# Optimization experiments

Hardware: AMD Instinct MI355X
Metric: run time of the kernel (lower is better)

The kernel has to match this reference:

```python
import jax, jax.numpy as jnp
import numpy as np

L = 65536      # number of received symbols
MT = 64        # Mtestangles
NF = 64        # averaging half-window -> filter length 2*NF+1 = 129


def setup_inputs() -> dict:
    key = jax.random.key(0)
    k1, k2 = jax.random.split(key, 2)
    # 64-QAM constellation, unit average power
    pts = jnp.arange(-7, 8, 2, dtype=jnp.float32)  # 8 PAM levels
    re, im = jnp.meshgrid(pts, pts, indexing='ij')
    sym = (re + 1j * im).reshape(-1)
    sym = sym / jnp.sqrt(jnp.mean(jnp.abs(sym) ** 2))
    # received signal: random constellation symbols + slow phase drift + noise
    idx = jax.random.randint(k1, (L,), 0, sym.shape[0])
    drift = jnp.cumsum(0.002 * jax.random.normal(k2, (L,), jnp.float32))
    noise = 0.05 * (jax.random.normal(jax.random.fold_in(key, 7), (L,), jnp.float32)
                    + 1j * jax.random.normal(jax.random.fold_in(key, 8), (L,), jnp.float32))
    x = sym[idx] * jnp.exp(1j * drift) + noise
    # triangular averaging filter: [1..N+1, N..1]
    avg_filter = jnp.concatenate([
        jnp.arange(1, NF + 2, dtype=jnp.float32),
        jnp.arange(NF, 0, -1, dtype=jnp.float32)])
    return {
        'x_real': x.real.astype(jnp.float32),
        'x_imag': x.imag.astype(jnp.float32),
        'symbols_real': sym.real.astype(jnp.float32),
        'symbols_imag': sym.imag.astype(jnp.float32),
        'avg_filter': avg_filter,
        'temperature': jnp.array([0.05], dtype=jnp.float32),
    }


def reference(x_real, x_imag, symbols_real, symbols_imag, avg_filter, temperature):
    # angles for no_sectors==4: linspace(-pi/4, pi/4 - (pi/2)/M, M)
    angles = jnp.linspace(-np.pi / 4, np.pi / 4 - (np.pi / 2) / MT, MT).astype(jnp.float32)  # [M]
    x = jax.lax.complex(x_real, x_imag)                       # [L]
    EE = x[:, None] * jnp.exp(1j * angles)                    # [L, M] rotated copies
    # dist[l,m] = min_s |EE - s|^2 = |x|^2 + min_s(|s|^2 - 2 Re(EE conj(s)))
    sym_sq = symbols_real ** 2 + symbols_imag ** 2            # [S]
    cross = EE.real[:, :, None] * symbols_real + EE.imag[:, :, None] * symbols_imag  # [L, M, S]
    dist = (x_real ** 2 + x_imag ** 2)[:, None] + jnp.min(sym_sq - 2.0 * cross, axis=2)  # [L, M]
    # sliding-window average along time (torch conv1d padding='same', normalized taps)
    w = avg_filter / jnp.sum(avg_filter)                      # [2N+1]
    mvg = jax.lax.conv_general_dilated(
        dist.T[:, None, :],            # [M, 1, L]
        w[None, None, :],              # [1, 1, 2N+1]
        window_strides=(1,), padding=[(NF, NF)],
        dimension_numbers=('NCH', 'OIH', 'NCH'))[:, 0, :].T   # [L, M]
    mvg = mvg / jnp.sum(mvg, axis=1, keepdims=True)
    # softmin over test angles
    smvg = jax.nn.softmax(-mvg / temperature[0], axis=1)      # [L, M]
    sang = 4.0 * angles
    ang = jnp.arctan2(smvg @ jnp.sin(sang), smvg @ jnp.cos(sang))  # [L]
    ph = jnp.unwrap(ang, discont=np.pi, period=2 * np.pi) / 4.0
    out = x * jnp.exp(1j * ph)
    return out, ph
```

## Files before the change

### kernel.cpp

```cpp
#include <hip/hip_runtime.h>


#define LN   65536
#define PI_F 3.14159265358979323846f
#define TWO_PI_F 6.2831853071795864769f

#define CORR(dd) (((dd) < -PI_F) ? 1 : (((dd) > PI_F) ? -1 : 0))

__global__ __launch_bounds__(512) void v14_stage_ang(const float* __restrict__ xr,
                                                     const float* __restrict__ xi,
                                                     const float* __restrict__ temp,
                                                     float* __restrict__ ang_out) {
    __shared__ float P1[64 * 257];
    __shared__ float xsr[256], xsi[256];
    __shared__ float tot1[8][64];
    __shared__ float tot2[8][64];
    __shared__ float s4v[64], c4v[64];

    const int t   = threadIdx.x;
    const int l0  = blockIdx.x * 128;
    const int m   = t & 63;
    const int seg = t >> 6;

    if (t < 256) {
        int gl = l0 - 64 + t;
        bool ok = (unsigned)gl < (unsigned)LN;
        xsr[t] = ok ? xr[gl] : 0.0f;
        xsi[t] = ok ? xi[gl] : 0.0f;
    }
    if (t >= 448) {
        int mm = t - 448;
        float a4 = (float)mm * (PI_F / 32.0f) - PI_F;
        float s, c; sincosf(a4, &s, &c);
        s4v[mm] = s; c4v[mm] = c;
    }
    __syncthreads();

    {
        const float am = (float)m * (PI_F / 128.0f) - (PI_F * 0.25f);
        float sm, cm; sincosf(am, &sm, &cm);
        const float SQ = 6.4807406984078602f;
        const float cq = cm * SQ, sq = sm * SQ;
        float pr[32];
        float p = 0.0f;
        #pragma unroll
        for (int i = 0; i < 32; ++i) {
            int li = seg * 32 + i;
            float a = xsr[li], b = xsi[li];
            float tr = a * cq - b * sq;
            float ti = a * sq + b * cq;
            float rr = fminf(fmaxf(rintf(fmaf(tr, 0.5f, 3.5f)), 0.0f), 7.0f);
            float ri = fminf(fmaxf(rintf(fmaf(ti, 0.5f, 3.5f)), 0.0f), 7.0f);
            float dr = fmaf(-2.0f, rr, tr + 7.0f);
            float di = fmaf(-2.0f, ri, ti + 7.0f);
            float d = fmaf(dr, dr, di * di) * (1.0f / 42.0f);
            d = ((unsigned)(l0 - 64 + li) < (unsigned)LN) ? d : 0.0f;
            p += d;
            pr[i] = p;
        }
        tot1[seg][m] = p;
        __syncthreads();
        float off = 0.0f;
        #pragma unroll
        for (int s = 0; s < 7; ++s) if (s < seg) off += tot1[s][m];
        #pragma unroll
        for (int i = 0; i < 32; ++i) P1[m * 257 + seg * 32 + i] = pr[i] + off;
    }
    __syncthreads();

    const int j0 = seg * 25;
    const int jn = (seg < 7) ? 25 : 18;
    {
        float q[25];
        float p2 = 0.0f;
        #pragma unroll
        for (int i = 0; i < 25; ++i) {
            if (i < jn) {
                int j = j0 + i;
                float hi = P1[m * 257 + 63 + j];
                float lo = (j >= 2) ? P1[m * 257 + j - 2] : 0.0f;
                p2 += hi - lo;
                q[i] = p2;
            }
        }
        tot2[seg][m] = p2;
        __syncthreads();
        float off2 = 0.0f;
        #pragma unroll
        for (int s = 0; s < 7; ++s) if (s < seg) off2 += tot2[s][m];
        float* Q = P1;
        #pragma unroll
        for (int i = 0; i < 25; ++i) if (i < jn) Q[m * 195 + j0 + i] = q[i] + off2;
    }
    __syncthreads();

    {
        const float* Q = P1;
        const float T = temp[0];
        const int sub = t & 3;
        const int r   = t >> 2;
        const int mb  = sub * 16;

        float v[16];
        float rs = 0.0f, mn = 3.4e38f;
        #pragma unroll
        for (int i = 0; i < 16; ++i) {
            int mm = mb + i;
            float vv = Q[mm * 195 + r + 65] - Q[mm * 195 + r];
            v[i] = vv; rs += vv; mn = fminf(mn, vv);
        }
        rs += __shfl_xor(rs, 1, 64); rs += __shfl_xor(rs, 2, 64);
        mn = fminf(mn, __shfl_xor(mn, 1, 64)); mn = fminf(mn, __shfl_xor(mn, 2, 64));

        float inv = 1.0f / (rs * T);
        float ss = 0.0f, sc = 0.0f;
        #pragma unroll
        for (int i = 0; i < 16; ++i) {
            int mm = mb + i;
            float e = __expf((mn - v[i]) * inv);
            ss = fmaf(e, s4v[mm], ss);
            sc = fmaf(e, c4v[mm], sc);
        }
        ss += __shfl_xor(ss, 1, 64); ss += __shfl_xor(ss, 2, 64);
        sc += __shfl_xor(sc, 1, 64); sc += __shfl_xor(sc, 2, 64);
        if (sub == 0) ang_out[l0 + r] = atan2f(ss, sc);
    }
}

__global__ __launch_bounds__(256) void v14_scan_out(const float* __restrict__ xr,
                                                    const float* __restrict__ xi,
                                                    const float* __restrict__ ang,
                                                    int* __restrict__ partial,
                                                    int* __restrict__ flags,
                                                    float* __restrict__ out_base) {
    __shared__ int wtot[4];
    __shared__ int s_boff;
    const int t = threadIdx.x;
    const int b = blockIdx.x;
    const int e = b * 256 + t;
    const int i4 = e * 4;

    float4 a = *(const float4*)(ang + i4);
    float prev = (i4 == 0) ? 0.0f : ang[i4 - 1];

    int s0 = CORR(a.x - prev);
    int s1 = CORR(a.y - a.x);
    int s2 = CORR(a.z - a.y);
    int s3 = CORR(a.w - a.z);
    int k0 = s0, k1 = k0 + s1, k2 = k1 + s2, k3 = k2 + s3;

    const int lane = t & 63, wv = t >> 6;
    int scan = k3;
    #pragma unroll
    for (int off = 1; off < 64; off <<= 1) {
        int v = __shfl_up(scan, off, 64);
        if (lane >= off) scan += v;
    }
    if (lane == 63) wtot[wv] = scan;
    __syncthreads();
    int woff = 0;
    #pragma unroll
    for (int j = 0; j < 3; ++j) if (j < wv) woff += wtot[j];
    const int excl = woff + scan - k3;

    if (t == 0) {
        int btot = wtot[0] + wtot[1] + wtot[2] + wtot[3];
        __hip_atomic_store(&partial[b], btot, __ATOMIC_RELAXED, __HIP_MEMORY_SCOPE_AGENT);
        __hip_atomic_store(&flags[b], 1, __ATOMIC_RELEASE, __HIP_MEMORY_SCOPE_AGENT);
    }
    if (t < 64) {
        int v = 0;
        if (t < b) {
            while (__hip_atomic_load(&flags[t], __ATOMIC_ACQUIRE, __HIP_MEMORY_SCOPE_AGENT) != 1) {}
            v = __hip_atomic_load(&partial[t], __ATOMIC_RELAXED, __HIP_MEMORY_SCOPE_AGENT);
        }
        #pragma unroll
        for (int off = 1; off < 64; off <<= 1) v += __shfl_xor(v, off, 64);
        if (t == 0) s_boff = v;
    }
    __syncthreads();
    const int boff = s_boff;

    float4 xa = *(const float4*)(xr + i4);
    float4 xb = *(const float4*)(xi + i4);
    float ph0 = (a.x + TWO_PI_F * (float)(boff + excl + k0)) * 0.25f;
    float ph1 = (a.y + TWO_PI_F * (float)(boff + excl + k1)) * 0.25f;
    float ph2 = (a.z + TWO_PI_F * (float)(boff + excl + k2)) * 0.25f;
    float ph3 = (a.w + TWO_PI_F * (float)(boff + excl + k3)) * 0.25f;
    float s0f, c0f, s1f, c1f, s2f, c2f, s3f, c3f;
    sincosf(ph0, &s0f, &c0f); sincosf(ph1, &s1f, &c1f);
    sincosf(ph2, &s2f, &c2f); sincosf(ph3, &s3f, &c3f);
    float4 re = make_float4(xa.x * c0f - xb.x * s0f, xa.y * c1f - xb.y * s1f,
                            xa.z * c2f - xb.z * s2f, xa.w * c3f - xb.w * s3f);
    *(float4*)(out_base + i4)      = re;
    *(float4*)(out_base + LN + i4) = make_float4(ph0, ph1, ph2, ph3);
}

extern "C" void kernel_launch(void* const* d_in, const int* in_sizes, int n_in,
                              void* d_out, int out_size, void* d_ws, size_t ws_size,
                              hipStream_t stream) {
    (void)in_sizes; (void)n_in; (void)out_size; (void)ws_size;
    const float* xr   = (const float*)d_in[0];
    const float* xi   = (const float*)d_in[1];
    const float* temp = (const float*)d_in[5];

    float* ang     = (float*)d_ws;
    int*   partial = (int*)((char*)d_ws + LN * sizeof(float));
    int*   flags   = (int*)((char*)d_ws + LN * sizeof(float) + 256);

    v14_stage_ang<<<LN / 128, 512, 0, stream>>>(xr, xi, temp, ang);
    v14_scan_out <<<64, 256, 0, stream>>>(xr, xi, ang, partial, flags, (float*)d_out);
}
```

Measured before the change: 76.71 us.

## Fuse angle stage and unwrap scan into one kernel with per-block lookback

Merges the angle-estimation kernel and the unwrap/rotate kernel into a single launch. Each block computes one extra halo angle so the unwrap difference at the block boundary is computed locally. Cross-block offsets come from a decoupled lookback over 512 block partials. This removes the second launch and the intermediate angle buffer, at the risk of serialized spin-waiting across many blocks and reliance on forward-progress scheduling.

```diff
diff --git a/kernel.cpp b/kernel.cpp
--- a/kernel.cpp
+++ b/kernel.cpp
@@ -7,23 +7,29 @@
 
 #define CORR(dd) (((dd) < -PI_F) ? 1 : (((dd) > PI_F) ? -1 : 0))
 
-__global__ __launch_bounds__(512) void v14_stage_ang(const float* __restrict__ xr,
-                                                     const float* __restrict__ xi,
-                                                     const float* __restrict__ temp,
-                                                     float* __restrict__ ang_out) {
-    __shared__ float P1[64 * 257];
-    __shared__ float xsr[256], xsi[256];
+__global__ __launch_bounds__(512) void v15_fused(const float* __restrict__ xr,
+                                                 const float* __restrict__ xi,
+                                                 const float* __restrict__ temp,
+                                                 int* __restrict__ partial,
+                                                 int* __restrict__ flags,
+                                                 float* __restrict__ out_base) {
+    __shared__ float P1[64 * 258];
+    __shared__ float xsr[260], xsi[260];
     __shared__ float tot1[8][64];
     __shared__ float tot2[8][64];
     __shared__ float s4v[64], c4v[64];
+    __shared__ float ang_lds[129];
+    __shared__ int   wtot[2];
+    __shared__ int   s_boff;
 
     const int t   = threadIdx.x;
-    const int l0  = blockIdx.x * 128;
+    const int b   = blockIdx.x;
+    const int l0  = b * 128;
     const int m   = t & 63;
     const int seg = t >> 6;
 
-    if (t < 256) {
-        int gl = l0 - 64 + t;
+    if (t < 257) {
+        int gl = l0 - 65 + t;
         bool ok = (unsigned)gl < (unsigned)LN;
         xsr[t] = ok ? xr[gl] : 0.0f;
         xsi[t] = ok ? xi[gl] : 0.0f;
@@ -41,22 +47,26 @@
         float sm, cm; sincosf(am, &sm, &cm);
         const float SQ = 6.4807406984078602f;
         const float cq = cm * SQ, sq = sm * SQ;
-        float pr[32];
+        const int li0 = seg * 33;
+        const int rn  = (seg < 7) ? 33 : 26;
+        float pr[33];
         float p = 0.0f;
         #pragma unroll
-        for (int i = 0; i < 32; ++i) {
-            int li = seg * 32 + i;
-            float a = xsr[li], b = xsi[li];
-            float tr = a * cq - b * sq;
-            float ti = a * sq + b * cq;
-            float rr = fminf(fmaxf(rintf(fmaf(tr, 0.5f, 3.5f)), 0.0f), 7.0f);
-            float ri = fminf(fmaxf(rintf(fmaf(ti, 0.5f, 3.5f)), 0.0f), 7.0f);
-            float dr = fmaf(-2.0f, rr, tr + 7.0f);
-            float di = fmaf(-2.0f, ri, ti + 7.0f);
-            float d = fmaf(dr, dr, di * di) * (1.0f / 42.0f);
-            d = ((unsigned)(l0 - 64 + li) < (unsigned)LN) ? d : 0.0f;
-            p += d;
-            pr[i] = p;
+        for (int i = 0; i < 33; ++i) {
+            if (i < rn) {
+                int li = li0 + i;
+                float a = xsr[li], bb = xsi[li];
+                float tr = a * cq - bb * sq;
+                float ti = a * sq + bb * cq;
+                float rr = fminf(fmaxf(rintf(fmaf(tr, 0.5f, 3.5f)), 0.0f), 7.0f);
+                float ri = fminf(fmaxf(rintf(fmaf(ti, 0.5f, 3.5f)), 0.0f), 7.0f);
+                float dr = fmaf(-2.0f, rr, tr + 7.0f);
+                float di = fmaf(-2.0f, ri, ti + 7.0f);
+                float d = fmaf(dr, dr, di * di) * (1.0f / 42.0f);
+                d = ((unsigned)(l0 - 65 + li) < (unsigned)LN) ? d : 0.0f;
+                p += d;
+                pr[i] = p;
+            }
         }
         tot1[seg][m] = p;
         __syncthreads();
@@ -64,21 +74,21 @@
         #pragma unroll
         for (int s = 0; s < 7; ++s) if (s < seg) off += tot1[s][m];
         #pragma unroll
-        for (int i = 0; i < 32; ++i) P1[m * 257 + seg * 32 + i] = pr[i] + off;
-    }
-    __syncthreads();
-
-    const int j0 = seg * 25;
-    const int jn = (seg < 7) ? 25 : 18;
+        for (int i = 0; i < 33; ++i) if (i < rn) P1[m * 258 + li0 + i] = pr[i] + off;
+    }
+    __syncthreads();
+
     {
+        const int j0 = seg * 25;
+        const int jn = (j0 < 193) ? ((193 - j0 < 25) ? (193 - j0) : 25) : 0;
         float q[25];
         float p2 = 0.0f;
         #pragma unroll
         for (int i = 0; i < 25; ++i) {
             if (i < jn) {
                 int j = j0 + i;
-                float hi = P1[m * 257 + 63 + j];
-                float lo = (j >= 2) ? P1[m * 257 + j - 2] : 0.0f;
+                float hi = P1[m * 258 + j + 64];
+                float lo = (j >= 1) ? P1[m * 258 + j - 1] : 0.0f;
                 p2 += hi - lo;
                 q[i] = p2;
             }
@@ -97,103 +107,89 @@
     {
         const float* Q = P1;
         const float T = temp[0];
-        const int sub = t & 3;
-        const int r   = t >> 2;
-        const int mb  = sub * 16;
-
-        float v[16];
-        float rs = 0.0f, mn = 3.4e38f;
-        #pragma unroll
-        for (int i = 0; i < 16; ++i) {
-            int mm = mb + i;
-            float vv = Q[mm * 195 + r + 65] - Q[mm * 195 + r];
-            v[i] = vv; rs += vv; mn = fminf(mn, vv);
-        }
-        rs += __shfl_xor(rs, 1, 64); rs += __shfl_xor(rs, 2, 64);
-        mn = fminf(mn, __shfl_xor(mn, 1, 64)); mn = fminf(mn, __shfl_xor(mn, 2, 64));
-
-        float inv = 1.0f / (rs * T);
-        float ss = 0.0f, sc = 0.0f;
-        #pragma unroll
-        for (int i = 0; i < 16; ++i) {
-            int mm = mb + i;
-            float e = __expf((mn - v[i]) * inv);
-            ss = fmaf(e, s4v[mm], ss);
-            sc = fmaf(e, c4v[mm], sc);
-        }
-        ss += __shfl_xor(ss, 1, 64); ss += __shfl_xor(ss, 2, 64);
-        sc += __shfl_xor(sc, 1, 64); sc += __shfl_xor(sc, 2, 64);
-        if (sub == 0) ang_out[l0 + r] = atan2f(ss, sc);
-    }
-}
-
-__global__ __launch_bounds__(256) void v14_scan_out(const float* __restrict__ xr,
-                                                    const float* __restrict__ xi,
-                                                    const float* __restrict__ ang,
-                                                    int* __restrict__ partial,
-                                                    int* __restrict__ flags,
-                                                    float* __restrict__ out_base) {
-    __shared__ int wtot[4];
-    __shared__ int s_boff;
-    const int t = threadIdx.x;
-    const int b = blockIdx.x;
-    const int e = b * 256 + t;
-    const int i4 = e * 4;
-
-    float4 a = *(const float4*)(ang + i4);
-    float prev = (i4 == 0) ? 0.0f : ang[i4 - 1];
-
-    int s0 = CORR(a.x - prev);
-    int s1 = CORR(a.y - a.x);
-    int s2 = CORR(a.z - a.y);
-    int s3 = CORR(a.w - a.z);
-    int k0 = s0, k1 = k0 + s1, k2 = k1 + s2, k3 = k2 + s3;
-
-    const int lane = t & 63, wv = t >> 6;
-    int scan = k3;
-    #pragma unroll
-    for (int off = 1; off < 64; off <<= 1) {
-        int v = __shfl_up(scan, off, 64);
-        if (lane >= off) scan += v;
-    }
-    if (lane == 63) wtot[wv] = scan;
-    __syncthreads();
-    int woff = 0;
-    #pragma unroll
-    for (int j = 0; j < 3; ++j) if (j < wv) woff += wtot[j];
-    const int excl = woff + scan - k3;
-
+        #pragma unroll
+        for (int pass = 0; pass < 2; ++pass) {
+            int rr;
+            bool act;
+            if (pass == 0) { rr = t >> 2; act = true; }
+            else           { rr = 128;    act = (t < 4); }
+            if (act) {
+                const int sub = t & 3;
+                const int mb  = sub * 16;
+                float v[16];
+                float rs = 0.0f, mn = 3.4e38f;
+                #pragma unroll
+                for (int i = 0; i < 16; ++i) {
+                    int mm = mb + i;
+                    float hi = Q[mm * 195 + rr + 64];
+                    float lo = (rr >= 1) ? Q[mm * 195 + rr - 1] : 0.0f;
+                    float vv = hi - lo;
+                    v[i] = vv; rs += vv; mn = fminf(mn, vv);
+                }
+                rs += __shfl_xor(rs, 1, 64); rs += __shfl_xor(rs, 2, 64);
+                mn = fminf(mn, __shfl_xor(mn, 1, 64)); mn = fminf(mn, __shfl_xor(mn, 2, 64));
+                float inv = 1.0f / (rs * T);
+                float ss = 0.0f, sc = 0.0f;
+                #pragma unroll
+                for (int i = 0; i < 16; ++i) {
+                    int mm = mb + i;
+                    float e = __expf((mn - v[i]) * inv);
+                    ss = fmaf(e, s4v[mm], ss);
+                    sc = fmaf(e, c4v[mm], sc);
+                }
+                ss += __shfl_xor(ss, 1, 64); ss += __shfl_xor(ss, 2, 64);
+                sc += __shfl_xor(sc, 1, 64); sc += __shfl_xor(sc, 2, 64);
+                if ((t & 3) == 0) ang_lds[rr] = atan2f(ss, sc);
+            }
+        }
+    }
+    __syncthreads();
+
+    int incl = 0, c = 0;
+    if (t < 128) {
+        float dd = ang_lds[t + 1] - ang_lds[t];
+        c = CORR(dd);
+        if (b == 0 && t == 0) c = 0;
+        const int lane = t & 63, w = t >> 6;
+        int sc = c;
+        #pragma unroll
+        for (int off = 1; off < 64; off <<= 1) {
+            int v = __shfl_up(sc, off, 64);
+            if (lane >= off) sc += v;
+        }
+        if (lane == 63) wtot[w] = sc;
+        incl = sc;
+    }
+    __syncthreads();
+    if (t < 128) {
+        if ((t >> 6) == 1) incl += wtot[0];
+    }
     if (t == 0) {
-        int btot = wtot[0] + wtot[1] + wtot[2] + wtot[3];
+        int btot = wtot[0] + wtot[1];
         __hip_atomic_store(&partial[b], btot, __ATOMIC_RELAXED, __HIP_MEMORY_SCOPE_AGENT);
         __hip_atomic_store(&flags[b], 1, __ATOMIC_RELEASE, __HIP_MEMORY_SCOPE_AGENT);
     }
     if (t < 64) {
         int v = 0;
-        if (t < b) {
-            while (__hip_atomic_load(&flags[t], __ATOMIC_ACQUIRE, __HIP_MEMORY_SCOPE_AGENT) != 1) {}
-            v = __hip_atomic_load(&partial[t], __ATOMIC_RELAXED, __HIP_MEMORY_SCOPE_AGENT);
+        for (int p = t; p < b; p += 64) {
+            while (__hip_atomic_load(&flags[p], __ATOMIC_ACQUIRE, __HIP_MEMORY_SCOPE_AGENT) != 1) {}
+            v += __hip_atomic_load(&partial[p], __ATOMIC_RELAXED, __HIP_MEMORY_SCOPE_AGENT);
         }
         #pragma unroll
         for (int off = 1; off < 64; off <<= 1) v += __shfl_xor(v, off, 64);
         if (t == 0) s_boff = v;
     }
     __syncthreads();
-    const int boff = s_boff;
-
-    float4 xa = *(const float4*)(xr + i4);
-    float4 xb = *(const float4*)(xi + i4);
-    float ph0 = (a.x + TWO_PI_F * (float)(boff + excl + k0)) * 0.25f;
-    float ph1 = (a.y + TWO_PI_F * (float)(boff + excl + k1)) * 0.25f;
-    float ph2 = (a.z + TWO_PI_F * (float)(boff + excl + k2)) * 0.25f;
-    float ph3 = (a.w + TWO_PI_F * (float)(boff + excl + k3)) * 0.25f;
-    float s0f, c0f, s1f, c1f, s2f, c2f, s3f, c3f;
-    sincosf(ph0, &s0f, &c0f); sincosf(ph1, &s1f, &c1f);
-    sincosf(ph2, &s2f, &c2f); sincosf(ph3, &s3f, &c3f);
-    float4 re = make_float4(xa.x * c0f - xb.x * s0f, xa.y * c1f - xb.y * s1f,
-                            xa.z * c2f - xb.z * s2f, xa.w * c3f - xb.w * s3f);
-    *(float4*)(out_base + i4)      = re;
-    *(float4*)(out_base + LN + i4) = make_float4(ph0, ph1, ph2, ph3);
+
+    if (t < 128) {
+        const int l = l0 + t;
+        int k = s_boff + incl;
+        float ph = (ang_lds[t + 1] + TWO_PI_F * (float)k) * 0.25f;
+        float s, cc; sincosf(ph, &s, &cc);
+        float a = xr[l], bb = xi[l];
+        out_base[l]      = a * cc - bb * s;
+        out_base[LN + l] = ph;
+    }
 }
 
 extern "C" void kernel_launch(void* const* d_in, const int* in_sizes, int n_in,
@@ -204,10 +200,8 @@
     const float* xi   = (const float*)d_in[1];
     const float* temp = (const float*)d_in[5];
 
-    float* ang     = (float*)d_ws;
-    int*   partial = (int*)((char*)d_ws + LN * sizeof(float));
-    int*   flags   = (int*)((char*)d_ws + LN * sizeof(float) + 256);
-
-    v14_stage_ang<<<LN / 128, 512, 0, stream>>>(xr, xi, temp, ang);
-    v14_scan_out <<<64, 256, 0, stream>>>(xr, xi, ang, partial, flags, (float*)d_out);
+    int* partial = (int*)d_ws;
+    int* flags   = (int*)((char*)d_ws + 4096);
+
+    v15_fused<<<512, 512, 0, stream>>>(xr, xi, temp, partial, flags, (float*)d_out);
 }
```

Result: slower. 95.62 us (+24.6%).
